# Kernel optimization log

Measured on AMD Instinct MI355X. Metric: run time of the kernel, lower is better.

Reference implementation:

```python
import jax, jax.numpy as jnp
import numpy as np

IN_CHANNELS = 2  # density + 1 value channel
OUT_CHANNELS = 64
INIT_LENGTH_SCALE = 0.03125


def setup_inputs() -> dict:
    key = jax.random.key(0)
    ks = jax.random.split(key, 5)
    B, N_IN, N_OUT = 8, 1024, 4096
    # locations in roughly [-2, 2]
    x = jax.random.uniform(ks[0], (B, N_IN, 2), jnp.float32, -2.0, 2.0)
    y = jax.random.normal(ks[1], (B, N_IN, 1), jnp.float32)
    t = jax.random.uniform(ks[2], (B, N_OUT, 2), jnp.float32, -2.0, 2.0)
    # learned params
    sigma = jnp.full((IN_CHANNELS,), np.log(INIT_LENGTH_SCALE), jnp.float32)
    W = jax.random.normal(ks[3], (OUT_CHANNELS, IN_CHANNELS), jnp.float32) / jnp.sqrt(IN_CHANNELS)
    b = jnp.zeros((OUT_CHANNELS,), jnp.float32)
    return {"x": x, "y": y, "t": t, "sigma": sigma, "W": W, "b": b}


def reference(x, y, t, sigma, W, b):
    # pairwise squared distances over 2D coords: (B, n_in, n_out)
    dists = ((x[:, :, None, 0] - t[:, None, :, 0]) ** 2
             + (x[:, :, None, 1] - t[:, None, :, 1]) ** 2)
    scales = jnp.exp(sigma)  # (C,) with C = in_channels = 2
    # RBF weights per channel: (B, n_in, n_out, C)
    wt = jnp.exp(-0.5 * dists[..., None] / scales ** 2)
    B, n_in, _ = x.shape
    density = jnp.ones((B, n_in, 1), x.dtype)
    dens_y = jnp.concatenate([density, y], axis=2)  # (B, n_in, C)
    # weighted sum over context points: (B, n_out, C)
    y_out = jnp.einsum('bnc,bnmc->bmc', dens_y, wt)
    dens, conv = y_out[..., :1], y_out[..., 1:]
    feat = jnp.concatenate([dens, conv / (dens + 1e-8)], axis=-1)  # (B, n_out, C)
    # pointwise linear to out_channels
    return jnp.einsum('bmc,oc->bmo', feat, W) + b
```

## Files before the change

kernel.cpp:

```cpp
#include <hip/hip_runtime.h>


#define OUTC 64
#define MB   128
#define NW   16

typedef __attribute__((ext_vector_type(2))) float f32x2;

__global__ __launch_bounds__(1024, 4) void convdeepset_kernel(
    const float* __restrict__ x,
    const float* __restrict__ y,
    const float* __restrict__ t,
    const float* __restrict__ sigma,
    const float* __restrict__ W,
    const float* __restrict__ bias,
    float* __restrict__ out)
{
    __shared__ float4 pk[1024];
    __shared__ float  dens_part[NW*MB];
    __shared__ float  conv_part[NW*MB];
    __shared__ float  sums[2*MB];
    __shared__ float  dens_tot[MB];
    __shared__ float  ratio[MB];

    const int tid = threadIdx.x;
    const int b   = blockIdx.x >> 5;
    const int m0  = (blockIdx.x & 31) * MB;

    const float log2e = 1.44269504088896340736f;
    const float k0 = -0.5f * __expf(-2.0f * sigma[0]) * log2e;
    const float k1 = -0.5f * __expf(-2.0f * sigma[1]) * log2e;
    const float s0 = sqrtf(-k0);
    const float r  = k1 / k0;

    {
        const float2 xv = ((const float2*)(x + (size_t)b * 2048))[tid];
        const float  yv = y[(size_t)b * 1024 + tid];
        const float sx = xv.x * s0, sy = xv.y * s0;
        pk[tid] = make_float4(sx + sx, sy + sy,
                              -fmaf(sx, sx, sy * sy), yv);
    }

    const int wave = tid >> 6;
    const int lane = tid & 63;
    const float2* tg = (const float2*)(t + ((size_t)b * 4096 + m0) * 2);
    const float2 ta = tg[lane];
    const float2 tb = tg[64 + lane];
    f32x2 u2, v2, cm2;
    u2.x = ta.x * s0;  u2.y = tb.x * s0;
    v2.x = ta.y * s0;  v2.y = tb.y * s0;
    cm2.x = -fmaf(u2.x, u2.x, v2.x * v2.x);
    cm2.y = -fmaf(u2.y, u2.y, v2.y * v2.y);

    __syncthreads();

    f32x2 dacc = {0.f, 0.f}, cacc = {0.f, 0.f};
    const int ibeg = wave * 64;

    if (r == 1.0f) {
        #pragma unroll 4
        for (int i = ibeg; i < ibeg + 64; ++i) {
            const float4 p = pk[i];
            f32x2 arg = cm2 + p.z;
            arg = __builtin_elementwise_fma((f32x2)p.x, u2, arg);
            arg = __builtin_elementwise_fma((f32x2)p.y, v2, arg);
            f32x2 e;
            e.x = __builtin_amdgcn_exp2f(arg.x);
            e.y = __builtin_amdgcn_exp2f(arg.y);
            dacc += e;
            cacc = __builtin_elementwise_fma((f32x2)p.w, e, cacc);
        }
    } else {
        #pragma unroll 2
        for (int i = ibeg; i < ibeg + 64; ++i) {
            const float4 p = pk[i];
            f32x2 arg = cm2 + p.z;
            arg = __builtin_elementwise_fma((f32x2)p.x, u2, arg);
            arg = __builtin_elementwise_fma((f32x2)p.y, v2, arg);
            f32x2 e, er;
            e.x  = __builtin_amdgcn_exp2f(arg.x);
            e.y  = __builtin_amdgcn_exp2f(arg.y);
            er.x = __builtin_amdgcn_exp2f(arg.x * r);
            er.y = __builtin_amdgcn_exp2f(arg.y * r);
            dacc += e;
            cacc = __builtin_elementwise_fma((f32x2)p.w, er, cacc);
        }
    }

    dens_part[wave * MB + lane]      = dacc.x;
    dens_part[wave * MB + 64 + lane] = dacc.y;
    conv_part[wave * MB + lane]      = cacc.x;
    conv_part[wave * MB + 64 + lane] = cacc.y;
    __syncthreads();

    if (tid < 2 * MB) {
        const int m = tid & (MB - 1);
        const float* src = (tid < MB) ? dens_part : conv_part;
        float s = 0.f;
        #pragma unroll
        for (int w = 0; w < NW; ++w) s += src[w * MB + m];
        sums[tid] = s;
    }
    __syncthreads();
    if (tid < MB) {
        float dt = sums[tid];
        dens_tot[tid] = dt;
        ratio[tid]    = sums[MB + tid] / (dt + 1e-8f);
    }
    __syncthreads();

    const int o = tid & 63;
    const int g = tid >> 6;
    const float w0 = W[o * 2 + 0];
    const float w1 = W[o * 2 + 1];
    const float bo = bias[o];
    float* outb = out + ((size_t)b * 4096 + m0) * OUTC;
    #pragma unroll
    for (int i = 0; i < 8; ++i) {
        int mm = g * 8 + i;
        outb[mm * OUTC + o] = fmaf(dens_tot[mm], w0, fmaf(ratio[mm], w1, bo));
    }
}

extern "C" void kernel_launch(void* const* d_in, const int* in_sizes, int n_in,
                              void* d_out, int out_size, void* d_ws, size_t ws_size,
                              hipStream_t stream) {
    const float* x     = (const float*)d_in[0];
    const float* y     = (const float*)d_in[1];
    const float* t     = (const float*)d_in[2];
    const float* sigma = (const float*)d_in[3];
    const float* W     = (const float*)d_in[4];
    const float* bias  = (const float*)d_in[5];
    float* out = (float*)d_out;

    convdeepset_kernel<<<dim3(256), dim3(1024), 0, stream>>>(
        x, y, t, sigma, W, bias, out);
}
```

Before: 72.06 us.

## Bin targets spatially and cull context points outside the RBF cutoff

A new pre-pass kernel sorts each batch's targets into an 8x8 serpentine grid of spatial cells, writing a target order to workspace. The main kernel then handles spatially coherent tiles of 128 targets and computes their bounding box. It compacts into shared memory only the context points within a margin where exp2 of the argument stays above about 2^-150. This skips exponentials whose results would underflow to zero. The cost is an extra launch, ballot-based compaction, dynamic loop bounds with possible imbalance across waves, and scattered output writes through the permutation.

```diff
diff --git a/kernel.cpp b/kernel.cpp
--- a/kernel.cpp
+++ b/kernel.cpp
@@ -6,6 +6,50 @@
 #define NW   16
 
 typedef __attribute__((ext_vector_type(2))) float f32x2;
+
+__global__ __launch_bounds__(1024) void bin_targets(
+    const float* __restrict__ t,
+    int* __restrict__ torder)
+{
+    const int b   = blockIdx.x;
+    const int tid = threadIdx.x;
+    __shared__ int hist[64];
+    __shared__ int base[64];
+    if (tid < 64) hist[tid] = 0;
+    __syncthreads();
+
+    int cid[4];
+    #pragma unroll
+    for (int k = 0; k < 4; ++k) {
+        const int m = tid + k * 1024;
+        const float2 tv = ((const float2*)(t + (size_t)b * 8192))[m];
+        int cx = (int)((tv.x + 2.0f) * 2.0f); cx = min(max(cx, 0), 7);
+        int cy = (int)((tv.y + 2.0f) * 2.0f); cy = min(max(cy, 0), 7);
+        const int c = cy * 8 + ((cy & 1) ? (7 - cx) : cx);
+        cid[k] = c;
+        atomicAdd(&hist[c], 1);
+    }
+    __syncthreads();
+
+    if (tid < 64) {
+        const int v = hist[tid];
+        int inc = v;
+        #pragma unroll
+        for (int off = 1; off < 64; off <<= 1) {
+            const int u = __shfl_up(inc, off);
+            if (tid >= off) inc += u;
+        }
+        base[tid] = inc - v;
+    }
+    __syncthreads();
+
+    #pragma unroll
+    for (int k = 0; k < 4; ++k) {
+        const int m = tid + k * 1024;
+        const int pos = atomicAdd(&base[cid[k]], 1);
+        torder[(size_t)b * 4096 + pos] = m;
+    }
+}
 
 __global__ __launch_bounds__(1024, 4) void convdeepset_kernel(
     const float* __restrict__ x,
@@ -14,53 +58,89 @@
     const float* __restrict__ sigma,
     const float* __restrict__ W,
     const float* __restrict__ bias,
+    const int* __restrict__ torder,
     float* __restrict__ out)
 {
-    __shared__ float4 pk[1024];
+    __shared__ float4 cs[1024];
     __shared__ float  dens_part[NW*MB];
     __shared__ float  conv_part[NW*MB];
     __shared__ float  sums[2*MB];
     __shared__ float  dens_tot[MB];
     __shared__ float  ratio[MB];
-
-    const int tid = threadIdx.x;
-    const int b   = blockIdx.x >> 5;
-    const int m0  = (blockIdx.x & 31) * MB;
+    __shared__ float2 stt[MB];
+    __shared__ int    tor[MB];
+    __shared__ int    wcnt[NW];
+
+    const int tid  = threadIdx.x;
+    const int b    = blockIdx.x >> 5;
+    const int m0   = (blockIdx.x & 31) * MB;
+    const int wave = tid >> 6;
+    const int lane = tid & 63;
 
     const float log2e = 1.44269504088896340736f;
     const float k0 = -0.5f * __expf(-2.0f * sigma[0]) * log2e;
     const float k1 = -0.5f * __expf(-2.0f * sigma[1]) * log2e;
     const float s0 = sqrtf(-k0);
     const float r  = k1 / k0;
-
+    const float marg = sqrtf(150.0f / fminf(r, 1.0f));
+
+    float sx, sy;
+    float4 myrec;
     {
         const float2 xv = ((const float2*)(x + (size_t)b * 2048))[tid];
         const float  yv = y[(size_t)b * 1024 + tid];
-        const float sx = xv.x * s0, sy = xv.y * s0;
-        pk[tid] = make_float4(sx + sx, sy + sy,
-                              -fmaf(sx, sx, sy * sy), yv);
-    }
-
-    const int wave = tid >> 6;
-    const int lane = tid & 63;
-    const float2* tg = (const float2*)(t + ((size_t)b * 4096 + m0) * 2);
-    const float2 ta = tg[lane];
-    const float2 tb = tg[64 + lane];
+        sx = xv.x * s0; sy = xv.y * s0;
+        myrec = make_float4(sx + sx, sy + sy, -fmaf(sx, sx, sy * sy), yv);
+    }
+
+    if (tid < MB) {
+        const int im = torder[(size_t)b * 4096 + m0 + tid];
+        tor[tid] = im;
+        const float2 tv = ((const float2*)(t + (size_t)b * 8192))[im];
+        stt[tid] = make_float2(tv.x * s0, tv.y * s0);
+    }
+    __syncthreads();
+
+    const float2 ta = stt[lane];
+    const float2 tb = stt[64 + lane];
+    float mnx = fminf(ta.x, tb.x), mxx = fmaxf(ta.x, tb.x);
+    float mny = fminf(ta.y, tb.y), mxy = fmaxf(ta.y, tb.y);
+    #pragma unroll
+    for (int off = 32; off; off >>= 1) {
+        mnx = fminf(mnx, __shfl_xor(mnx, off));
+        mxx = fmaxf(mxx, __shfl_xor(mxx, off));
+        mny = fminf(mny, __shfl_xor(mny, off));
+        mxy = fmaxf(mxy, __shfl_xor(mxy, off));
+    }
+    mnx -= marg; mxx += marg; mny -= marg; mxy += marg;
+
+    const bool keep = (sx >= mnx) && (sx <= mxx) && (sy >= mny) && (sy <= mxy);
+    const unsigned long long bal = __ballot(keep);
+    if (lane == 0) wcnt[wave] = __popcll(bal);
+    __syncthreads();
+    int basew = 0, K = 0;
+    #pragma unroll
+    for (int w2 = 0; w2 < NW; ++w2) {
+        const int c = wcnt[w2];
+        K += c;
+        if (w2 < wave) basew += c;
+    }
+    if (keep)
+        cs[basew + __popcll(bal & ((1ull << lane) - 1ull))] = myrec;
+    __syncthreads();
+
     f32x2 u2, v2, cm2;
-    u2.x = ta.x * s0;  u2.y = tb.x * s0;
-    v2.x = ta.y * s0;  v2.y = tb.y * s0;
-    cm2.x = -fmaf(u2.x, u2.x, v2.x * v2.x);
-    cm2.y = -fmaf(u2.y, u2.y, v2.y * v2.y);
-
-    __syncthreads();
+    u2.x = ta.x;  u2.y = tb.x;
+    v2.x = ta.y;  v2.y = tb.y;
+    cm2.x = -fmaf(ta.x, ta.x, ta.y * ta.y);
+    cm2.y = -fmaf(tb.x, tb.x, tb.y * tb.y);
 
     f32x2 dacc = {0.f, 0.f}, cacc = {0.f, 0.f};
-    const int ibeg = wave * 64;
 
     if (r == 1.0f) {
-        #pragma unroll 4
-        for (int i = ibeg; i < ibeg + 64; ++i) {
-            const float4 p = pk[i];
+        #pragma unroll 2
+        for (int i = wave; i < K; i += NW) {
+            const float4 p = cs[i];
             f32x2 arg = cm2 + p.z;
             arg = __builtin_elementwise_fma((f32x2)p.x, u2, arg);
             arg = __builtin_elementwise_fma((f32x2)p.y, v2, arg);
@@ -72,8 +152,8 @@
         }
     } else {
         #pragma unroll 2
-        for (int i = ibeg; i < ibeg + 64; ++i) {
-            const float4 p = pk[i];
+        for (int i = wave; i < K; i += NW) {
+            const float4 p = cs[i];
             f32x2 arg = cm2 + p.z;
             arg = __builtin_elementwise_fma((f32x2)p.x, u2, arg);
             arg = __builtin_elementwise_fma((f32x2)p.y, v2, arg);
@@ -103,7 +183,7 @@
     }
     __syncthreads();
     if (tid < MB) {
-        float dt = sums[tid];
+        const float dt = sums[tid];
         dens_tot[tid] = dt;
         ratio[tid]    = sums[MB + tid] / (dt + 1e-8f);
     }
@@ -114,11 +194,12 @@
     const float w0 = W[o * 2 + 0];
     const float w1 = W[o * 2 + 1];
     const float bo = bias[o];
-    float* outb = out + ((size_t)b * 4096 + m0) * OUTC;
+    float* outb = out + (size_t)b * 4096 * OUTC;
     #pragma unroll
     for (int i = 0; i < 8; ++i) {
-        int mm = g * 8 + i;
-        outb[mm * OUTC + o] = fmaf(dens_tot[mm], w0, fmaf(ratio[mm], w1, bo));
+        const int mm = g * 8 + i;
+        outb[(size_t)tor[mm] * OUTC + o] =
+            fmaf(dens_tot[mm], w0, fmaf(ratio[mm], w1, bo));
     }
 }
 
@@ -132,7 +213,9 @@
     const float* W     = (const float*)d_in[4];
     const float* bias  = (const float*)d_in[5];
     float* out = (float*)d_out;
-
+    int* torder = (int*)d_ws;
+
+    bin_targets<<<dim3(8), dim3(1024), 0, stream>>>(t, torder);
     convdeepset_kernel<<<dim3(256), dim3(1024), 0, stream>>>(
-        x, y, t, sigma, W, bias, out);
+        x, y, t, sigma, W, bias, torder, out);
 }
```

After: 74.90 us. 3.9% more time.

## Split work into smaller 256-thread blocks of 32 targets each

Applied to the files above, without the earlier changes.

Blocks now cover 32 target points with 256 threads instead of 128 targets with 1024 threads, giving 1024 blocks in place of 256. Each wave splits into four quarter-groups of 16 lanes that stride through the context points, so a block still sweeps all 1024 of them. The partial-sum buffers are padded to avoid bank conflicts, and the two reduction passes are merged into one. The aim is to fill the GPU's compute units more evenly. The cost is that every block has to reload and preprocess all context points, which adds four times the global loads and shared-memory setup.

```diff
diff --git a/kernel.cpp b/kernel.cpp
--- a/kernel.cpp
+++ b/kernel.cpp
@@ -2,12 +2,12 @@
 
 
 #define OUTC 64
-#define MB   128
-#define NW   16
+#define MB   32
+#define NROW 16
 
 typedef __attribute__((ext_vector_type(2))) float f32x2;
 
-__global__ __launch_bounds__(1024, 4) void convdeepset_kernel(
+__global__ __launch_bounds__(256, 4) void convdeepset_kernel(
     const float* __restrict__ x,
     const float* __restrict__ y,
     const float* __restrict__ t,
@@ -17,15 +17,14 @@
     float* __restrict__ out)
 {
     __shared__ float4 pk[1024];
-    __shared__ float  dens_part[NW*MB];
-    __shared__ float  conv_part[NW*MB];
-    __shared__ float  sums[2*MB];
+    __shared__ float  dens_part[NROW*(MB+1)];
+    __shared__ float  conv_part[NROW*(MB+1)];
     __shared__ float  dens_tot[MB];
     __shared__ float  ratio[MB];
 
     const int tid = threadIdx.x;
-    const int b   = blockIdx.x >> 5;
-    const int m0  = (blockIdx.x & 31) * MB;
+    const int b   = blockIdx.x >> 7;
+    const int m0  = (blockIdx.x & 127) * MB;
 
     const float log2e = 1.44269504088896340736f;
     const float k0 = -0.5f * __expf(-2.0f * sigma[0]) * log2e;
@@ -33,19 +32,23 @@
     const float s0 = sqrtf(-k0);
     const float r  = k1 / k0;
 
-    {
-        const float2 xv = ((const float2*)(x + (size_t)b * 2048))[tid];
-        const float  yv = y[(size_t)b * 1024 + tid];
+    #pragma unroll
+    for (int k = 0; k < 4; ++k) {
+        const int i = tid + k * 256;
+        const float2 xv = ((const float2*)(x + (size_t)b * 2048))[i];
+        const float  yv = y[(size_t)b * 1024 + i];
         const float sx = xv.x * s0, sy = xv.y * s0;
-        pk[tid] = make_float4(sx + sx, sy + sy,
-                              -fmaf(sx, sx, sy * sy), yv);
+        pk[i] = make_float4(sx + sx, sy + sy, -fmaf(sx, sx, sy * sy), yv);
     }
 
     const int wave = tid >> 6;
     const int lane = tid & 63;
+    const int q    = lane >> 4;
+    const int ml   = lane & 15;
+
     const float2* tg = (const float2*)(t + ((size_t)b * 4096 + m0) * 2);
-    const float2 ta = tg[lane];
-    const float2 tb = tg[64 + lane];
+    const float2 ta = tg[ml];
+    const float2 tb = tg[16 + ml];
     f32x2 u2, v2, cm2;
     u2.x = ta.x * s0;  u2.y = tb.x * s0;
     v2.x = ta.y * s0;  v2.y = tb.y * s0;
@@ -55,12 +58,12 @@
     __syncthreads();
 
     f32x2 dacc = {0.f, 0.f}, cacc = {0.f, 0.f};
-    const int ibeg = wave * 64;
+    const int nbase = wave * 256 + q;
 
     if (r == 1.0f) {
         #pragma unroll 4
-        for (int i = ibeg; i < ibeg + 64; ++i) {
-            const float4 p = pk[i];
+        for (int i = 0; i < 64; ++i) {
+            const float4 p = pk[nbase + i * 4];
             f32x2 arg = cm2 + p.z;
             arg = __builtin_elementwise_fma((f32x2)p.x, u2, arg);
             arg = __builtin_elementwise_fma((f32x2)p.y, v2, arg);
@@ -72,8 +75,8 @@
         }
     } else {
         #pragma unroll 2
-        for (int i = ibeg; i < ibeg + 64; ++i) {
-            const float4 p = pk[i];
+        for (int i = 0; i < 64; ++i) {
+            const float4 p = pk[nbase + i * 4];
             f32x2 arg = cm2 + p.z;
             arg = __builtin_elementwise_fma((f32x2)p.x, u2, arg);
             arg = __builtin_elementwise_fma((f32x2)p.y, v2, arg);
@@ -87,25 +90,22 @@
         }
     }
 
-    dens_part[wave * MB + lane]      = dacc.x;
-    dens_part[wave * MB + 64 + lane] = dacc.y;
-    conv_part[wave * MB + lane]      = cacc.x;
-    conv_part[wave * MB + 64 + lane] = cacc.y;
+    const int row = (wave << 2) | q;
+    dens_part[row * (MB + 1) + ml]      = dacc.x;
+    dens_part[row * (MB + 1) + 16 + ml] = dacc.y;
+    conv_part[row * (MB + 1) + ml]      = cacc.x;
+    conv_part[row * (MB + 1) + 16 + ml] = cacc.y;
     __syncthreads();
 
-    if (tid < 2 * MB) {
-        const int m = tid & (MB - 1);
-        const float* src = (tid < MB) ? dens_part : conv_part;
-        float s = 0.f;
+    if (tid < MB) {
+        float sd = 0.f, sc = 0.f;
         #pragma unroll
-        for (int w = 0; w < NW; ++w) s += src[w * MB + m];
-        sums[tid] = s;
-    }
-    __syncthreads();
-    if (tid < MB) {
-        float dt = sums[tid];
-        dens_tot[tid] = dt;
-        ratio[tid]    = sums[MB + tid] / (dt + 1e-8f);
+        for (int w = 0; w < NROW; ++w) {
+            sd += dens_part[w * (MB + 1) + tid];
+            sc += conv_part[w * (MB + 1) + tid];
+        }
+        dens_tot[tid] = sd;
+        ratio[tid]    = sc / (sd + 1e-8f);
     }
     __syncthreads();
 
@@ -117,7 +117,7 @@
     float* outb = out + ((size_t)b * 4096 + m0) * OUTC;
     #pragma unroll
     for (int i = 0; i < 8; ++i) {
-        int mm = g * 8 + i;
+        const int mm = g * 8 + i;
         outb[mm * OUTC + o] = fmaf(dens_tot[mm], w0, fmaf(ratio[mm], w1, bo));
     }
 }
@@ -133,6 +133,6 @@
     const float* bias  = (const float*)d_in[5];
     float* out = (float*)d_out;
 
-    convdeepset_kernel<<<dim3(256), dim3(1024), 0, stream>>>(
+    convdeepset_kernel<<<dim3(1024), dim3(256), 0, stream>>>(
         x, y, t, sigma, W, bias, out);
 }
```

Measured after the change: 71.65 us. Within noise of the previous version (-0.6%).
